# Performance work log

Measured on AMD Instinct MI355X. Metric: run time of the kernel, lower is better.

## Reference

```python
import math
import jax, jax.numpy as jnp
import numpy as np


def _skew(X, pad_value):
    # shift every row i one step right relative to row i-1: [B,M,L] -> [B,M,M+L]
    B, M, L = X.shape
    X = jnp.pad(X, ((0, 0), (0, 0), (0, M + 1)), constant_values=pad_value)
    X = X.reshape(B, -1)[:, :-M]
    return X.reshape(B, M, M + L)


def _unskew(X):
    # reverse of _skew: [B,M,M+L] -> [B,M,L]
    B, M, ML = X.shape
    L = ML - M
    X = X.reshape(B, -1)
    X = jnp.pad(X, ((0, 0), (0, M)))
    X = X.reshape(B, M, M + L + 1)
    return X[:, :, :L]


def setup_inputs() -> dict:
    key0 = jax.random.key(0)
    k1, k2, k3, k4 = jax.random.split(key0, 4)
    BH, M, D = 64, 1024, 64          # batch*heads, block len, head dim
    L = 1024                          # attn_span
    return {
        "query": jax.random.normal(k1, (BH, M, D), dtype=jnp.float32),
        "key": jax.random.normal(k2, (BH, M + L, D), dtype=jnp.float32),
        "value": jax.random.normal(k3, (BH, M + L, D), dtype=jnp.float32),
        "key_pe": jax.random.normal(k4, (1, D, L), dtype=jnp.float32),
    }


def reference(query, key, value, key_pe):
    hidden_size = query.shape[-1]
    # content scores: [BH, M, M+L] -> banded [BH, M, L]
    attn_cont = _unskew(jnp.matmul(query, jnp.swapaxes(key, -1, -2)))
    # relative position scores: [BH, M, L] (key_pe broadcasts over batch)
    attn_pos = jnp.matmul(query, key_pe)
    attn = (attn_cont + attn_pos) / math.sqrt(hidden_size)
    attn = jax.nn.softmax(attn, axis=-1)
    # dropout p=0.0 -> identity
    attn_skew = _skew(attn, 0.0)          # [BH, M, M+L]
    out = jnp.matmul(attn_skew, value)    # [BH, M, D]
    return out
```

## Files before the change

### kernel.cpp

```cpp
#include <hip/hip_runtime.h>
#include <hip/hip_bf16.h>


typedef __attribute__((ext_vector_type(8))) short bf16x8;
typedef __attribute__((ext_vector_type(4))) short bf16x4;
typedef __attribute__((ext_vector_type(4))) float f32x4;

#define BHN   64
#define MQ    1024
#define DH    64
#define LS    1024
#define NKEY  2048
#define NTILE 17

#define SZ_PE  ((size_t)LS * DH * 2)
#define OFF_K  SZ_PE
#define SZ_K   ((size_t)BHN * NKEY * DH * 2)
#define OFF_V  (OFF_K + SZ_K)
#define SZ_V   ((size_t)BHN * DH * NKEY * 2)
#define WS_NEED (OFF_V + SZ_V)

#define SCL_LOG2E 0.18033688011112042f

__device__ __forceinline__ short f2bf(float f) {
  unsigned u = __float_as_uint(f);
  u += 0x7FFFu + ((u >> 16) & 1u);
  return (short)(u >> 16);
}
__device__ __forceinline__ float bf2f(short s) {
  return __uint_as_float(((unsigned)(unsigned short)s) << 16);
}

#if defined(__has_builtin)
#if __has_builtin(__builtin_amdgcn_cvt_pk_bf16_f32)
#define HAVE_CVT_PK 1
#endif
#if __has_builtin(__builtin_amdgcn_exp2f)
#define HAVE_EXP2 1
#endif
#endif

__device__ __forceinline__ float fast_exp2(float x) {
#ifdef HAVE_EXP2
  return __builtin_amdgcn_exp2f(x);
#else
  return __builtin_exp2f(x);
#endif
}

__device__ __forceinline__ unsigned pk2(float a, float b) {
#ifdef HAVE_CVT_PK
  auto r = __builtin_amdgcn_cvt_pk_bf16_f32(a, b);
  unsigned u;
  __builtin_memcpy(&u, &r, 4);
  return u;
#else
  return (unsigned)(unsigned short)f2bf(a) | ((unsigned)(unsigned short)f2bf(b) << 16);
#endif
}
__device__ __forceinline__ bf16x4 mk4(unsigned a, unsigned b) {
  union { unsigned u[2]; bf16x4 v; } z;
  z.u[0] = a; z.u[1] = b;
  return z.v;
}
__device__ __forceinline__ bf16x8 mk8(unsigned a, unsigned b, unsigned c, unsigned d) {
  union { unsigned u[4]; bf16x8 v; } z;
  z.u[0] = a; z.u[1] = b; z.u[2] = c; z.u[3] = d;
  return z.v;
}

__global__ __launch_bounds__(256)
void prep_fused(const float* __restrict__ pe, const float* __restrict__ K,
                const float* __restrict__ V, short* __restrict__ peT,
                short* __restrict__ Kb, short* __restrict__ Vb) {
  __shared__ short st[64 * 68];
  const int bx = blockIdx.x;
  if (bx < 256) {
    const int idx = bx * 256 + threadIdx.x;
    const int rel = idx >> 6, d = idx & 63;
    peT[rel * 64 + (((d >> 3) ^ (rel & 7)) * 8) + (d & 7)] = f2bf(pe[d * LS + rel]);
  } else if (bx < 2304) {
    const size_t i = ((size_t)(bx - 256) * 256 + threadIdx.x) * 16;
    const int row = (int)(i >> 6);
    const int c16 = (int)(i & 63);
    const float4 f0 = *(const float4*)(K + i);
    const float4 f1 = *(const float4*)(K + i + 4);
    const float4 f2 = *(const float4*)(K + i + 8);
    const float4 f3 = *(const float4*)(K + i + 12);
    const bf16x8 b0 = mk8(pk2(f0.x, f0.y), pk2(f0.z, f0.w), pk2(f1.x, f1.y), pk2(f1.z, f1.w));
    const bf16x8 b1 = mk8(pk2(f2.x, f2.y), pk2(f2.z, f2.w), pk2(f3.x, f3.y), pk2(f3.z, f3.w));
    const int s7 = row & 7;
    short* dst = Kb + (size_t)row * 64;
    *(bf16x8*)&dst[(((c16 >> 3))     ^ s7) * 8] = b0;
    *(bf16x8*)&dst[(((c16 >> 3) + 1) ^ s7) * 8] = b1;
  } else {
    const int b  = bx - 2304;
    const int bh = b >> 5, jt = b & 31;
    {
      const int r = threadIdx.x >> 2, cb = (threadIdx.x & 3) * 16;
      const float* src = V + ((size_t)bh * NKEY + jt * 64 + r) * DH + cb;
#pragma unroll
      for (int c = 0; c < 16; c += 8) {
        float4 f0 = *(const float4*)(src + c);
        float4 f1 = *(const float4*)(src + c + 4);
        *(bf16x8*)&st[r * 68 + cb + c] =
            mk8(pk2(f0.x, f0.y), pk2(f0.z, f0.w), pk2(f1.x, f1.y), pk2(f1.z, f1.w));
      }
    }
    __syncthreads();
    {
      const int d = threadIdx.x >> 2, kapb = (threadIdx.x & 3) * 16;
      __attribute__((aligned(16))) short tmp[16];
#pragma unroll
      for (int j = 0; j < 16; ++j) {
        const int kap = kapb + j;
        const int k   = (kap & 3) * 16 + (kap >> 2);
        tmp[j] = st[k * 68 + d];
      }
      short* dst = Vb + ((size_t)bh * DH + d) * NKEY + jt * 64 + kapb;
      *(bf16x8*)dst       = *(bf16x8*)&tmp[0];
      *(bf16x8*)(dst + 8) = *(bf16x8*)&tmp[8];
    }
  }
}

template <bool PRECONV>
__global__ __launch_bounds__(256, 4)
void seq_attn_kernel(const float* __restrict__ Qf, const float* __restrict__ Kf,
                     const float* __restrict__ Vf, const short* __restrict__ peT,
                     const short* __restrict__ Kb, const short* __restrict__ Vb,
                     float* __restrict__ Out) {
  __shared__ short sK[64 * 64];
  __shared__ short sPE[2 * 64 * 64];
  __shared__ short sV[64 * 64];
  __shared__ short sPA[64 * 64];

  const int tid  = threadIdx.x;
  const int w    = tid >> 6;
  const int lane = tid & 63;
  const int li   = lane & 15;
  const int quad = lane >> 4;
  const int linear = blockIdx.y * 16 + blockIdx.x;
  const int slot   = linear >> 3;
  const int bh     = (linear & 7) * 8 + (slot >> 4);
  const int i0     = (slot & 15) * 64;
  const int rbase  = w * 16 + quad * 4;

  bf16x8 aq[2];
  {
    const float* qp = Qf + (size_t)((bh * MQ + i0 + w * 16 + li) * DH) + quad * 8;
#pragma unroll
    for (int ks = 0; ks < 2; ++ks) {
      float4 f0 = *(const float4*)(qp + ks * 32);
      float4 f1 = *(const float4*)(qp + ks * 32 + 4);
      f0.x *= SCL_LOG2E; f0.y *= SCL_LOG2E; f0.z *= SCL_LOG2E; f0.w *= SCL_LOG2E;
      f1.x *= SCL_LOG2E; f1.y *= SCL_LOG2E; f1.z *= SCL_LOG2E; f1.w *= SCL_LOG2E;
      aq[ks] = mk8(pk2(f0.x, f0.y), pk2(f0.z, f0.w), pk2(f1.x, f1.y), pk2(f1.z, f1.w));
    }
  }

  float l_i[4] = {0.f, 0.f, 0.f, 0.f};
  f32x4 acco[4];
#pragma unroll
  for (int nt = 0; nt < 4; ++nt) acco[nt] = (f32x4){0.f, 0.f, 0.f, 0.f};

  f32x4 curPw[4];
  f32x4 prevw3 = (f32x4){0.f, 0.f, 0.f, 0.f};

  bf16x8 pfK0, pfK1, pfP0, pfP1, pfV0, pfV1;
  const short *pK, *pP, *pV0, *pV1;
  if constexpr (PRECONV) {
    pK = Kb + ((size_t)bh * NKEY + i0) * DH + tid * 8 + 1024;
    pP = peT + tid * 8 + 1024;
    const int d0 = tid >> 3;
    const int g0 = (tid & 7) ^ (d0 & 7);
    pV0 = Vb + ((size_t)bh * DH + d0) * NKEY + i0 + g0 * 8;
    pV1 = pV0 + (size_t)32 * NKEY;
    pfK0 = *(const bf16x8*)(pK - 1024);
    pfK1 = *(const bf16x8*)(pK + 1024);
    pfP0 = *(const bf16x8*)(pP - 1024);
    pfP1 = *(const bf16x8*)(pP + 1024);
    pfV0 = *(const bf16x8*)(pV0);
    pfV1 = *(const bf16x8*)(pV1);
    pK += 4096; pP += 4096; pV0 += 64; pV1 += 64;
  }

  for (int t = 0; t < NTILE; ++t) {
    __syncthreads();

    if constexpr (PRECONV) {
      *(bf16x8*)&sK[tid * 8]        = pfK0;
      *(bf16x8*)&sK[tid * 8 + 2048] = pfK1;
      if (t < NTILE - 1) {
        short* pe = sPE + (t & 1) * 4096;
        *(bf16x8*)&pe[tid * 8]        = pfP0;
        *(bf16x8*)&pe[tid * 8 + 2048] = pfP1;
      }
      *(bf16x8*)&sV[tid * 8]        = pfV0;
      *(bf16x8*)&sV[tid * 8 + 2048] = pfV1;
      if (t + 1 < NTILE) {
        pfK0 = *(const bf16x8*)(pK - 1024);
        pfK1 = *(const bf16x8*)(pK + 1024);
        pfV0 = *(const bf16x8*)(pV0);
        pfV1 = *(const bf16x8*)(pV1);
        pK += 4096; pV0 += 64; pV1 += 64;
        if (t + 1 < NTILE - 1) {
          pfP0 = *(const bf16x8*)(pP - 1024);
          pfP1 = *(const bf16x8*)(pP + 1024);
          pP += 4096;
        }
      }
      asm volatile("s_waitcnt lgkmcnt(0)" ::: "memory");
      __builtin_amdgcn_sched_barrier(0);
      __builtin_amdgcn_s_barrier();
      __builtin_amdgcn_sched_barrier(0);
    } else {
      const int j0 = i0 + t * 64;
      {
        const int srow = tid >> 2, l0 = tid & 3, sdb = l0 * 16;
        const float* src = Kf + (size_t)(bh * NKEY + j0 + srow) * DH + sdb;
        const float4 a0 = *(const float4*)(src + 0);
        const float4 a1 = *(const float4*)(src + 4);
        const float4 a2 = *(const float4*)(src + 8);
        const float4 a3 = *(const float4*)(src + 12);
        const bf16x8 b0 = mk8(pk2(a0.x, a0.y), pk2(a0.z, a0.w), pk2(a1.x, a1.y), pk2(a1.z, a1.w));
        const bf16x8 b1 = mk8(pk2(a2.x, a2.y), pk2(a2.z, a2.w), pk2(a3.x, a3.y), pk2(a3.z, a3.w));
        const int s7 = srow & 7;
        *(bf16x8*)&sK[srow * 64 + (((2 * l0)     ^ s7) * 8)] = b0;
        *(bf16x8*)&sK[srow * 64 + (((2 * l0 + 1) ^ s7) * 8)] = b1;
      }
      {
        const int vdb = (tid & 15) * 4, vkb = (tid >> 4) * 4;
        const float* src = Vf + (size_t)(bh * NKEY + j0 + vkb) * DH + vdb;
#pragma unroll
        for (int m = 0; m < 4; ++m) {
          const float4 rr = *(const float4*)(src + m * DH);
          const int k   = vkb + m;
          const int kap = (k & 15) * 4 + (k >> 4);
#pragma unroll
          for (int jj = 0; jj < 4; ++jj) {
            const int d = vdb + jj;
            const float fv = (jj == 0) ? rr.x : (jj == 1) ? rr.y : (jj == 2) ? rr.z : rr.w;
            sV[d * 64 + (((kap >> 3) ^ (d & 7)) * 8) + (kap & 7)] = f2bf(fv);
          }
        }
      }
      if (t < NTILE - 1) {
        const short* src = peT + (size_t)t * 64 * 64;
        short* db = sPE + (size_t)(t & 1) * 4096;
        *(bf16x8*)&db[tid * 16]     = *(const bf16x8*)(src + tid * 16);
        *(bf16x8*)&db[tid * 16 + 8] = *(const bf16x8*)(src + tid * 16 + 8);
      }
      __syncthreads();
    }

    __builtin_amdgcn_s_setprio(1);
#pragma unroll
    for (int m = 0; m < 4; ++m) {
      const int colIdx = 4 * t - w + m;
      const int base = ((colIdx >> 2) & 1) * 4096 + ((colIdx & 3) * 16 + li) * 64;
      f32x4 c = (f32x4){0.f, 0.f, 0.f, 0.f};
#pragma unroll
      for (int ks = 0; ks < 2; ++ks) {
        const int gs = (((ks * 4 + quad) ^ (li & 7)) * 8);
        const bf16x8 b = *(bf16x8*)&sPE[base + gs];
        c = __builtin_amdgcn_mfma_f32_16x16x32_bf16(aq[ks], b, c, 0, 0, 0);
      }
      curPw[m] = c;
    }

    f32x4 cs[4];
#pragma unroll
    for (int nt = 0; nt < 4; ++nt) {
      f32x4 c = (f32x4){0.f, 0.f, 0.f, 0.f};
#pragma unroll
      for (int ks = 0; ks < 2; ++ks) {
        const int gs = (((ks * 4 + quad) ^ (li & 7)) * 8);
        const bf16x8 b = *(bf16x8*)&sK[(nt * 16 + li) * 64 + gs];
        c = __builtin_amdgcn_mfma_f32_16x16x32_bf16(aq[ks], b, c, 0, 0, 0);
      }
      cs[nt] = c;
    }
    __builtin_amdgcn_s_setprio(0);

#pragma unroll
    for (int r = 0; r < 4; ++r) {
      const int e       = li - quad * 4 - r;
      const bool ge     = (e >= 0);
      const int srcLane = quad * 16 + (e & 15);
      const float shm = __shfl(prevw3[r], srcLane);
      const unsigned pk01 = pk2(curPw[0][r], curPw[1][r]);
      const unsigned pk23 = pk2(curPw[2][r], curPw[3][r]);
      const unsigned s01 = (unsigned)__shfl((int)pk01, srcLane);
      const unsigned s23 = (unsigned)__shfl((int)pk23, srcLane);
      const float sh0 = bf2f((short)(s01 & 0xffffu));
      const float sh1 = bf2f((short)(s01 >> 16));
      const float sh2 = bf2f((short)(s23 & 0xffffu));
      const float sh3 = bf2f((short)(s23 >> 16));
      const float pos0 = ge ? sh0 : shm;
      const float pos1 = ge ? sh1 : sh0;
      const float pos2 = ge ? sh2 : sh1;
      const float pos3 = ge ? sh3 : sh2;
      float p0 = fast_exp2(cs[0][r] + pos0);
      float p1 = fast_exp2(cs[1][r] + pos1);
      float p2 = fast_exp2(cs[2][r] + pos2);
      float p3 = fast_exp2(cs[3][r] + pos3);
      if (t == 0) {
        p0 = (0 > w || (0 == w && ge)) ? p0 : 0.f;
        p1 = (1 > w || (1 == w && ge)) ? p1 : 0.f;
        p2 = (2 > w || (2 == w && ge)) ? p2 : 0.f;
        p3 = (3 > w || (3 == w && ge)) ? p3 : 0.f;
      } else if (t == NTILE - 1) {
        p0 = (0 < w || (0 == w && !ge)) ? p0 : 0.f;
        p1 = (1 < w || (1 == w && !ge)) ? p1 : 0.f;
        p2 = (2 < w || (2 == w && !ge)) ? p2 : 0.f;
        p3 = (3 < w || (3 == w && !ge)) ? p3 : 0.f;
      }
      l_i[r] += (p0 + p1) + (p2 + p3);
      const int rowA = rbase + r;
      const bf16x4 pkv = mk4(pk2(p0, p1), pk2(p2, p3));
      *(bf16x4*)&sPA[rowA * 64 + (((li >> 1) ^ (rowA & 7)) * 8) + (li & 1) * 4] = pkv;
    }
    prevw3 = curPw[3];

    __builtin_amdgcn_s_setprio(1);
#pragma unroll
    for (int ks = 0; ks < 2; ++ks) {
      const int rowA = w * 16 + li;
      const bf16x8 ap =
          *(bf16x8*)&sPA[rowA * 64 + (((ks * 4 + quad) ^ (rowA & 7)) * 8)];
#pragma unroll
      for (int nt = 0; nt < 4; ++nt) {
        const int d  = nt * 16 + li;
        const int gs = (((ks * 4 + quad) ^ (d & 7)) * 8);
        const bf16x8 bv = *(bf16x8*)&sV[d * 64 + gs];
        acco[nt] = __builtin_amdgcn_mfma_f32_16x16x32_bf16(ap, bv, acco[nt], 0, 0, 0);
      }
    }
    __builtin_amdgcn_s_setprio(0);
  }

#pragma unroll
  for (int r = 0; r < 4; ++r) {
    float l = l_i[r];
    l += __shfl_xor(l, 1);
    l += __shfl_xor(l, 2);
    l += __shfl_xor(l, 4);
    l += __shfl_xor(l, 8);
    const float inv = 1.0f / l;
#pragma unroll
    for (int nt = 0; nt < 4; ++nt) {
      Out[(size_t)(bh * MQ + i0 + rbase + r) * DH + nt * 16 + li] = acco[nt][r] * inv;
    }
  }
}

extern "C" void kernel_launch(void* const* d_in, const int* in_sizes, int n_in,
                              void* d_out, int out_size, void* d_ws, size_t ws_size,
                              hipStream_t stream) {
  const float* q  = (const float*)d_in[0];
  const float* k  = (const float*)d_in[1];
  const float* v  = (const float*)d_in[2];
  const float* pe = (const float*)d_in[3];
  float* out = (float*)d_out;
  short* peT = (short*)d_ws;
  short* Kb  = (short*)((char*)d_ws + OFF_K);
  short* Vb  = (short*)((char*)d_ws + OFF_V);
  const bool preconv = ws_size >= WS_NEED;

  dim3 grid(MQ / 64, BHN);
  if (preconv) {
    prep_fused<<<4352, 256, 0, stream>>>(pe, k, v, peT, Kb, Vb);
    seq_attn_kernel<true><<<grid, 256, 0, stream>>>(q, k, v, peT, Kb, Vb, out);
  } else {
    prep_fused<<<256, 256, 0, stream>>>(pe, k, v, peT, Kb, Vb);
    seq_attn_kernel<false><<<grid, 256, 0, stream>>>(q, k, v, peT, Kb, Vb, out);
  }
}
```

Before: 171.3 us.

## Process two 64-row query groups per block to reuse K/V tiles

Each block now handles 128 query rows as two 64-row groups that share every loaded K and V tile, so the band loop runs 18 tiles instead of 17 per 64 rows. This roughly halves global K/V traffic per query row. The PE buffer becomes a 4-slot ring, the P staging buffer doubles, and the barrier moves to the start of each iteration. In exchange, register pressure rises (launch bounds drop to 2 blocks per CU), the grid halves to 512 blocks, and one extra masked tile adds wasted work per group.

```diff
diff --git a/kernel.cpp b/kernel.cpp
--- a/kernel.cpp
+++ b/kernel.cpp
@@ -11,7 +11,8 @@
 #define DH    64
 #define LS    1024
 #define NKEY  2048
-#define NTILE 17
+#define NT    18
+#define NPE   16
 
 #define SZ_PE  ((size_t)LS * DH * 2)
 #define OFF_K  SZ_PE
@@ -124,48 +125,99 @@
   }
 }
 
+__device__ __forceinline__ void softmax_band(
+    const f32x4* cs, const f32x4* cur, const f32x4& prev,
+    float (&l_acc)[4], short* sPA, const int rowbase, const int tt,
+    const int w, const int li, const int quad) {
+#pragma unroll
+  for (int r = 0; r < 4; ++r) {
+    const int e       = li - quad * 4 - r;
+    const bool ge     = (e >= 0);
+    const int srcLane = quad * 16 + (e & 15);
+    const float shm = __shfl(prev[r], srcLane);
+    const unsigned pk01 = pk2(cur[0][r], cur[1][r]);
+    const unsigned pk23 = pk2(cur[2][r], cur[3][r]);
+    const unsigned s01 = (unsigned)__shfl((int)pk01, srcLane);
+    const unsigned s23 = (unsigned)__shfl((int)pk23, srcLane);
+    const float sh0 = bf2f((short)(s01 & 0xffffu));
+    const float sh1 = bf2f((short)(s01 >> 16));
+    const float sh2 = bf2f((short)(s23 & 0xffffu));
+    const float sh3 = bf2f((short)(s23 >> 16));
+    const float pos0 = ge ? sh0 : shm;
+    const float pos1 = ge ? sh1 : sh0;
+    const float pos2 = ge ? sh2 : sh1;
+    const float pos3 = ge ? sh3 : sh2;
+    float p0 = fast_exp2(cs[0][r] + pos0);
+    float p1 = fast_exp2(cs[1][r] + pos1);
+    float p2 = fast_exp2(cs[2][r] + pos2);
+    float p3 = fast_exp2(cs[3][r] + pos3);
+    if (tt == 0) {
+      p0 = (0 > w || (0 == w && ge)) ? p0 : 0.f;
+      p1 = (1 > w || (1 == w && ge)) ? p1 : 0.f;
+      p2 = (2 > w || (2 == w && ge)) ? p2 : 0.f;
+      p3 = (3 > w || (3 == w && ge)) ? p3 : 0.f;
+    } else if (tt == 16) {
+      p0 = (0 < w || (0 == w && !ge)) ? p0 : 0.f;
+      p1 = (1 < w || (1 == w && !ge)) ? p1 : 0.f;
+      p2 = (2 < w || (2 == w && !ge)) ? p2 : 0.f;
+      p3 = (3 < w || (3 == w && !ge)) ? p3 : 0.f;
+    } else if ((unsigned)tt > 16u) {
+      p0 = 0.f; p1 = 0.f; p2 = 0.f; p3 = 0.f;
+    }
+    l_acc[r] += (p0 + p1) + (p2 + p3);
+    const int rowA = rowbase + w * 16 + quad * 4 + r;
+    const bf16x4 pkv = mk4(pk2(p0, p1), pk2(p2, p3));
+    *(bf16x4*)&sPA[rowA * 64 + (((li >> 1) ^ (rowA & 7)) * 8) + (li & 1) * 4] = pkv;
+  }
+}
+
 template <bool PRECONV>
-__global__ __launch_bounds__(256, 4)
+__global__ __launch_bounds__(256, 2)
 void seq_attn_kernel(const float* __restrict__ Qf, const float* __restrict__ Kf,
                      const float* __restrict__ Vf, const short* __restrict__ peT,
                      const short* __restrict__ Kb, const short* __restrict__ Vb,
                      float* __restrict__ Out) {
   __shared__ short sK[64 * 64];
-  __shared__ short sPE[2 * 64 * 64];
+  __shared__ short sPE[4 * 64 * 64];
   __shared__ short sV[64 * 64];
-  __shared__ short sPA[64 * 64];
+  __shared__ short sPA[128 * 64];
 
   const int tid  = threadIdx.x;
   const int w    = tid >> 6;
   const int lane = tid & 63;
   const int li   = lane & 15;
   const int quad = lane >> 4;
-  const int linear = blockIdx.y * 16 + blockIdx.x;
-  const int slot   = linear >> 3;
-  const int bh     = (linear & 7) * 8 + (slot >> 4);
-  const int i0     = (slot & 15) * 64;
+  const int linear = blockIdx.y * 8 + blockIdx.x;
+  const int within = linear >> 3;
+  const int bh     = (linear & 7) * 8 + (within >> 3);
+  const int i0     = (within & 7) * 128;
   const int rbase  = w * 16 + quad * 4;
 
-  bf16x8 aq[2];
-  {
-    const float* qp = Qf + (size_t)((bh * MQ + i0 + w * 16 + li) * DH) + quad * 8;
+  bf16x8 aq0[2], aq1[2];
+#pragma unroll
+  for (int g = 0; g < 2; ++g) {
+    const float* qp = Qf + (size_t)((bh * MQ + i0 + g * 64 + w * 16 + li) * DH) + quad * 8;
 #pragma unroll
     for (int ks = 0; ks < 2; ++ks) {
       float4 f0 = *(const float4*)(qp + ks * 32);
       float4 f1 = *(const float4*)(qp + ks * 32 + 4);
       f0.x *= SCL_LOG2E; f0.y *= SCL_LOG2E; f0.z *= SCL_LOG2E; f0.w *= SCL_LOG2E;
       f1.x *= SCL_LOG2E; f1.y *= SCL_LOG2E; f1.z *= SCL_LOG2E; f1.w *= SCL_LOG2E;
-      aq[ks] = mk8(pk2(f0.x, f0.y), pk2(f0.z, f0.w), pk2(f1.x, f1.y), pk2(f1.z, f1.w));
-    }
-  }
-
-  float l_i[4] = {0.f, 0.f, 0.f, 0.f};
-  f32x4 acco[4];
-#pragma unroll
-  for (int nt = 0; nt < 4; ++nt) acco[nt] = (f32x4){0.f, 0.f, 0.f, 0.f};
-
-  f32x4 curPw[4];
-  f32x4 prevw3 = (f32x4){0.f, 0.f, 0.f, 0.f};
+      const bf16x8 v = mk8(pk2(f0.x, f0.y), pk2(f0.z, f0.w), pk2(f1.x, f1.y), pk2(f1.z, f1.w));
+      if (g == 0) aq0[ks] = v; else aq1[ks] = v;
+    }
+  }
+
+  float l0[4] = {0.f, 0.f, 0.f, 0.f};
+  float l1[4] = {0.f, 0.f, 0.f, 0.f};
+  f32x4 acco0[4], acco1[4];
+#pragma unroll
+  for (int nt = 0; nt < 4; ++nt) {
+    acco0[nt] = (f32x4){0.f, 0.f, 0.f, 0.f};
+    acco1[nt] = (f32x4){0.f, 0.f, 0.f, 0.f};
+  }
+  f32x4 prev0 = (f32x4){0.f, 0.f, 0.f, 0.f};
+  f32x4 prev1 = (f32x4){0.f, 0.f, 0.f, 0.f};
 
   bf16x8 pfK0, pfK1, pfP0, pfP1, pfV0, pfV1;
   const short *pK, *pP, *pV0, *pV1;
@@ -185,26 +237,28 @@
     pK += 4096; pP += 4096; pV0 += 64; pV1 += 64;
   }
 
-  for (int t = 0; t < NTILE; ++t) {
-    __syncthreads();
-
+  for (int t = 0; t < NT; ++t) {
     if constexpr (PRECONV) {
+      asm volatile("s_waitcnt lgkmcnt(0)" ::: "memory");
+      __builtin_amdgcn_sched_barrier(0);
+      __builtin_amdgcn_s_barrier();
+      __builtin_amdgcn_sched_barrier(0);
       *(bf16x8*)&sK[tid * 8]        = pfK0;
       *(bf16x8*)&sK[tid * 8 + 2048] = pfK1;
-      if (t < NTILE - 1) {
-        short* pe = sPE + (t & 1) * 4096;
-        *(bf16x8*)&pe[tid * 8]        = pfP0;
-        *(bf16x8*)&pe[tid * 8 + 2048] = pfP1;
+      if (t < NPE) {
+        short* ped = sPE + (size_t)(t & 3) * 4096;
+        *(bf16x8*)&ped[tid * 8]        = pfP0;
+        *(bf16x8*)&ped[tid * 8 + 2048] = pfP1;
       }
       *(bf16x8*)&sV[tid * 8]        = pfV0;
       *(bf16x8*)&sV[tid * 8 + 2048] = pfV1;
-      if (t + 1 < NTILE) {
+      if (t + 1 < NT) {
         pfK0 = *(const bf16x8*)(pK - 1024);
         pfK1 = *(const bf16x8*)(pK + 1024);
         pfV0 = *(const bf16x8*)(pV0);
         pfV1 = *(const bf16x8*)(pV1);
         pK += 4096; pV0 += 64; pV1 += 64;
-        if (t + 1 < NTILE - 1) {
+        if (t + 1 < NPE) {
           pfP0 = *(const bf16x8*)(pP - 1024);
           pfP1 = *(const bf16x8*)(pP + 1024);
           pP += 4096;
@@ -215,9 +269,10 @@
       __builtin_amdgcn_s_barrier();
       __builtin_amdgcn_sched_barrier(0);
     } else {
+      __syncthreads();
       const int j0 = i0 + t * 64;
       {
-        const int srow = tid >> 2, l0 = tid & 3, sdb = l0 * 16;
+        const int srow = tid >> 2, lx = tid & 3, sdb = lx * 16;
         const float* src = Kf + (size_t)(bh * NKEY + j0 + srow) * DH + sdb;
         const float4 a0 = *(const float4*)(src + 0);
         const float4 a1 = *(const float4*)(src + 4);
@@ -226,8 +281,8 @@
         const bf16x8 b0 = mk8(pk2(a0.x, a0.y), pk2(a0.z, a0.w), pk2(a1.x, a1.y), pk2(a1.z, a1.w));
         const bf16x8 b1 = mk8(pk2(a2.x, a2.y), pk2(a2.z, a2.w), pk2(a3.x, a3.y), pk2(a3.z, a3.w));
         const int s7 = srow & 7;
-        *(bf16x8*)&sK[srow * 64 + (((2 * l0)     ^ s7) * 8)] = b0;
-        *(bf16x8*)&sK[srow * 64 + (((2 * l0 + 1) ^ s7) * 8)] = b1;
+        *(bf16x8*)&sK[srow * 64 + (((2 * lx)     ^ s7) * 8)] = b0;
+        *(bf16x8*)&sK[srow * 64 + (((2 * lx + 1) ^ s7) * 8)] = b1;
       }
       {
         const int vdb = (tid & 15) * 4, vkb = (tid >> 4) * 4;
@@ -245,96 +300,79 @@
           }
         }
       }
-      if (t < NTILE - 1) {
+      if (t < NPE) {
         const short* src = peT + (size_t)t * 64 * 64;
-        short* db = sPE + (size_t)(t & 1) * 4096;
+        short* db = sPE + (size_t)(t & 3) * 4096;
         *(bf16x8*)&db[tid * 16]     = *(const bf16x8*)(src + tid * 16);
         *(bf16x8*)&db[tid * 16 + 8] = *(const bf16x8*)(src + tid * 16 + 8);
       }
       __syncthreads();
     }
 
+    f32x4 cur0[4], cur1[4];
     __builtin_amdgcn_s_setprio(1);
 #pragma unroll
     for (int m = 0; m < 4; ++m) {
       const int colIdx = 4 * t - w + m;
-      const int base = ((colIdx >> 2) & 1) * 4096 + ((colIdx & 3) * 16 + li) * 64;
+      const int base = ((colIdx >> 2) & 3) * 4096 + ((colIdx & 3) * 16 + li) * 64;
       f32x4 c = (f32x4){0.f, 0.f, 0.f, 0.f};
 #pragma unroll
       for (int ks = 0; ks < 2; ++ks) {
         const int gs = (((ks * 4 + quad) ^ (li & 7)) * 8);
         const bf16x8 b = *(bf16x8*)&sPE[base + gs];
-        c = __builtin_amdgcn_mfma_f32_16x16x32_bf16(aq[ks], b, c, 0, 0, 0);
-      }
-      curPw[m] = c;
-    }
-
-    f32x4 cs[4];
+        c = __builtin_amdgcn_mfma_f32_16x16x32_bf16(aq0[ks], b, c, 0, 0, 0);
+      }
+      cur0[m] = c;
+    }
+#pragma unroll
+    for (int m = 0; m < 4; ++m) {
+      const int colIdx = 4 * t - w + m - 4;
+      const int base = ((colIdx >> 2) & 3) * 4096 + ((colIdx & 3) * 16 + li) * 64;
+      f32x4 c = (f32x4){0.f, 0.f, 0.f, 0.f};
+#pragma unroll
+      for (int ks = 0; ks < 2; ++ks) {
+        const int gs = (((ks * 4 + quad) ^ (li & 7)) * 8);
+        const bf16x8 b = *(bf16x8*)&sPE[base + gs];
+        c = __builtin_amdgcn_mfma_f32_16x16x32_bf16(aq1[ks], b, c, 0, 0, 0);
+      }
+      cur1[m] = c;
+    }
+
+    f32x4 cs0[4], cs1[4];
 #pragma unroll
     for (int nt = 0; nt < 4; ++nt) {
-      f32x4 c = (f32x4){0.f, 0.f, 0.f, 0.f};
+      f32x4 c0 = (f32x4){0.f, 0.f, 0.f, 0.f};
+      f32x4 c1 = (f32x4){0.f, 0.f, 0.f, 0.f};
 #pragma unroll
       for (int ks = 0; ks < 2; ++ks) {
         const int gs = (((ks * 4 + quad) ^ (li & 7)) * 8);
         const bf16x8 b = *(bf16x8*)&sK[(nt * 16 + li) * 64 + gs];
-        c = __builtin_amdgcn_mfma_f32_16x16x32_bf16(aq[ks], b, c, 0, 0, 0);
-      }
-      cs[nt] = c;
+        c0 = __builtin_amdgcn_mfma_f32_16x16x32_bf16(aq0[ks], b, c0, 0, 0, 0);
+        c1 = __builtin_amdgcn_mfma_f32_16x16x32_bf16(aq1[ks], b, c1, 0, 0, 0);
+      }
+      cs0[nt] = c0; cs1[nt] = c1;
     }
     __builtin_amdgcn_s_setprio(0);
 
-#pragma unroll
-    for (int r = 0; r < 4; ++r) {
-      const int e       = li - quad * 4 - r;
-      const bool ge     = (e >= 0);
-      const int srcLane = quad * 16 + (e & 15);
-      const float shm = __shfl(prevw3[r], srcLane);
-      const unsigned pk01 = pk2(curPw[0][r], curPw[1][r]);
-      const unsigned pk23 = pk2(curPw[2][r], curPw[3][r]);
-      const unsigned s01 = (unsigned)__shfl((int)pk01, srcLane);
-      const unsigned s23 = (unsigned)__shfl((int)pk23, srcLane);
-      const float sh0 = bf2f((short)(s01 & 0xffffu));
-      const float sh1 = bf2f((short)(s01 >> 16));
-      const float sh2 = bf2f((short)(s23 & 0xffffu));
-      const float sh3 = bf2f((short)(s23 >> 16));
-      const float pos0 = ge ? sh0 : shm;
-      const float pos1 = ge ? sh1 : sh0;
-      const float pos2 = ge ? sh2 : sh1;
-      const float pos3 = ge ? sh3 : sh2;
-      float p0 = fast_exp2(cs[0][r] + pos0);
-      float p1 = fast_exp2(cs[1][r] + pos1);
-      float p2 = fast_exp2(cs[2][r] + pos2);
-      float p3 = fast_exp2(cs[3][r] + pos3);
-      if (t == 0) {
-        p0 = (0 > w || (0 == w && ge)) ? p0 : 0.f;
-        p1 = (1 > w || (1 == w && ge)) ? p1 : 0.f;
-        p2 = (2 > w || (2 == w && ge)) ? p2 : 0.f;
-        p3 = (3 > w || (3 == w && ge)) ? p3 : 0.f;
-      } else if (t == NTILE - 1) {
-        p0 = (0 < w || (0 == w && !ge)) ? p0 : 0.f;
-        p1 = (1 < w || (1 == w && !ge)) ? p1 : 0.f;
-        p2 = (2 < w || (2 == w && !ge)) ? p2 : 0.f;
-        p3 = (3 < w || (3 == w && !ge)) ? p3 : 0.f;
-      }
-      l_i[r] += (p0 + p1) + (p2 + p3);
-      const int rowA = rbase + r;
-      const bf16x4 pkv = mk4(pk2(p0, p1), pk2(p2, p3));
-      *(bf16x4*)&sPA[rowA * 64 + (((li >> 1) ^ (rowA & 7)) * 8) + (li & 1) * 4] = pkv;
-    }
-    prevw3 = curPw[3];
+    softmax_band(cs0, cur0, prev0, l0, sPA, 0,  t,     w, li, quad);
+    softmax_band(cs1, cur1, prev1, l1, sPA, 64, t - 1, w, li, quad);
+    prev0 = cur0[3];
+    prev1 = cur1[3];
 
     __builtin_amdgcn_s_setprio(1);
 #pragma unroll
     for (int ks = 0; ks < 2; ++ks) {
-      const int rowA = w * 16 + li;
-      const bf16x8 ap =
-          *(bf16x8*)&sPA[rowA * 64 + (((ks * 4 + quad) ^ (rowA & 7)) * 8)];
+      const int rA0 = w * 16 + li;
+      const int rA1 = rA0 + 64;
+      const bf16x8 ap0 = *(bf16x8*)&sPA[rA0 * 64 + (((ks * 4 + quad) ^ (rA0 & 7)) * 8)];
+      const bf16x8 ap1 = *(bf16x8*)&sPA[rA1 * 64 + (((ks * 4 + quad) ^ (rA1 & 7)) * 8)];
 #pragma unroll
       for (int nt = 0; nt < 4; ++nt) {
         const int d  = nt * 16 + li;
         const int gs = (((ks * 4 + quad) ^ (d & 7)) * 8);
         const bf16x8 bv = *(bf16x8*)&sV[d * 64 + gs];
-        acco[nt] = __builtin_amdgcn_mfma_f32_16x16x32_bf16(ap, bv, acco[nt], 0, 0, 0);
+        acco0[nt] = __builtin_amdgcn_mfma_f32_16x16x32_bf16(ap0, bv, acco0[nt], 0, 0, 0);
+        acco1[nt] = __builtin_amdgcn_mfma_f32_16x16x32_bf16(ap1, bv, acco1[nt], 0, 0, 0);
       }
     }
     __builtin_amdgcn_s_setprio(0);
@@ -342,7 +380,7 @@
 
 #pragma unroll
   for (int r = 0; r < 4; ++r) {
-    float l = l_i[r];
+    float l = l0[r];
     l += __shfl_xor(l, 1);
     l += __shfl_xor(l, 2);
     l += __shfl_xor(l, 4);
@@ -350,7 +388,20 @@
     const float inv = 1.0f / l;
 #pragma unroll
     for (int nt = 0; nt < 4; ++nt) {
-      Out[(size_t)(bh * MQ + i0 + rbase + r) * DH + nt * 16 + li] = acco[nt][r] * inv;
+      Out[(size_t)(bh * MQ + i0 + rbase + r) * DH + nt * 16 + li] = acco0[nt][r] * inv;
+    }
+  }
+#pragma unroll
+  for (int r = 0; r < 4; ++r) {
+    float l = l1[r];
+    l += __shfl_xor(l, 1);
+    l += __shfl_xor(l, 2);
+    l += __shfl_xor(l, 4);
+    l += __shfl_xor(l, 8);
+    const float inv = 1.0f / l;
+#pragma unroll
+    for (int nt = 0; nt < 4; ++nt) {
+      Out[(size_t)(bh * MQ + i0 + 64 + rbase + r) * DH + nt * 16 + li] = acco1[nt][r] * inv;
     }
   }
 }
@@ -368,7 +419,7 @@
   short* Vb  = (short*)((char*)d_ws + OFF_V);
   const bool preconv = ws_size >= WS_NEED;
 
-  dim3 grid(MQ / 64, BHN);
+  dim3 grid(8, BHN);
   if (preconv) {
     prep_fused<<<4352, 256, 0, stream>>>(pe, k, v, peT, Kb, Vb);
     seq_attn_kernel<true><<<grid, 256, 0, stream>>>(q, k, v, peT, Kb, Vb, out);
```

Measured after the change: 175.4 us. 2.4% more time.

## Software-pipeline QK of next tile with softmax/PV of previous, drop PE LDS staging

Applied to the files above, without the earlier changes.

Restructures the main loop into two-tile steps so the QK and position-score MFMAs for one tile are issued before the softmax and PV of the previous tile, giving cross-tile overlap. The position-embedding B operand is now read straight from global memory (peT) instead of being staged in LDS, and the P matrix reuses the sK buffer. V is double-buffered instead. The exchange is more barriers per tile, higher register pressure from two live score sets, and uncoalesced-ish global reads of peT that rely on the cache.

```diff
diff --git a/kernel.cpp b/kernel.cpp
--- a/kernel.cpp
+++ b/kernel.cpp
@@ -68,6 +68,14 @@
   z.u[0] = a; z.u[1] = b; z.u[2] = c; z.u[3] = d;
   return z.v;
 }
+
+#define RAWBAR()                                          \
+  do {                                                    \
+    asm volatile("s_waitcnt lgkmcnt(0)" ::: "memory");    \
+    __builtin_amdgcn_sched_barrier(0);                    \
+    __builtin_amdgcn_s_barrier();                         \
+    __builtin_amdgcn_sched_barrier(0);                    \
+  } while (0)
 
 __global__ __launch_bounds__(256)
 void prep_fused(const float* __restrict__ pe, const float* __restrict__ K,
@@ -124,6 +132,110 @@
   }
 }
 
+__device__ __forceinline__ void qk_tile(const short* sK, const bf16x8 (&aq)[2],
+                                        int li, int quad, f32x4 (&cs)[4]) {
+  const int g0 = ((quad) ^ (li & 7)) * 8;
+  const int g1 = ((4 + quad) ^ (li & 7)) * 8;
+#pragma unroll
+  for (int nt = 0; nt < 4; ++nt) {
+    const int row = (nt * 16 + li) * 64;
+    f32x4 c = (f32x4){0.f, 0.f, 0.f, 0.f};
+    c = __builtin_amdgcn_mfma_f32_16x16x32_bf16(aq[0], *(const bf16x8*)&sK[row + g0], c, 0, 0, 0);
+    c = __builtin_amdgcn_mfma_f32_16x16x32_bf16(aq[1], *(const bf16x8*)&sK[row + g1], c, 0, 0, 0);
+    cs[nt] = c;
+  }
+}
+
+__device__ __forceinline__ void pe_tile(const short* __restrict__ peT,
+                                        const bf16x8 (&aq)[2], int t, int w,
+                                        int li, int quad, unsigned (&pk)[8]) {
+  const int g0 = ((quad) ^ (li & 7)) * 8;
+  const int g1 = ((4 + quad) ^ (li & 7)) * 8;
+  f32x4 cur[4];
+#pragma unroll
+  for (int m = 0; m < 4; ++m) {
+    int cidx = 4 * t - w + m;
+    cidx = cidx < 0 ? 0 : (cidx > 63 ? 63 : cidx);
+    const short* p = peT + (size_t)(cidx * 16 + li) * 64;
+    f32x4 c = (f32x4){0.f, 0.f, 0.f, 0.f};
+    c = __builtin_amdgcn_mfma_f32_16x16x32_bf16(aq[0], *(const bf16x8*)(p + g0), c, 0, 0, 0);
+    c = __builtin_amdgcn_mfma_f32_16x16x32_bf16(aq[1], *(const bf16x8*)(p + g1), c, 0, 0, 0);
+    cur[m] = c;
+  }
+#pragma unroll
+  for (int r = 0; r < 4; ++r) {
+    pk[r * 2]     = pk2(cur[0][r], cur[1][r]);
+    pk[r * 2 + 1] = pk2(cur[2][r], cur[3][r]);
+  }
+}
+
+__device__ __forceinline__ void softmax_tile(const f32x4 (&cs)[4], const unsigned (&pk)[8],
+                                             f32x4& prevw3, float (&l_i)[4],
+                                             bf16x4 (&pkv)[4], int tt, int w,
+                                             int li, int quad) {
+#pragma unroll
+  for (int r = 0; r < 4; ++r) {
+    const int e       = li - quad * 4 - r;
+    const bool ge     = (e >= 0);
+    const int srcLane = quad * 16 + (e & 15);
+    const float shm = __shfl(prevw3[r], srcLane);
+    const unsigned s01 = (unsigned)__shfl((int)pk[r * 2], srcLane);
+    const unsigned s23 = (unsigned)__shfl((int)pk[r * 2 + 1], srcLane);
+    const float sh0 = bf2f((short)(s01 & 0xffffu));
+    const float sh1 = bf2f((short)(s01 >> 16));
+    const float sh2 = bf2f((short)(s23 & 0xffffu));
+    const float sh3 = bf2f((short)(s23 >> 16));
+    const float pos0 = ge ? sh0 : shm;
+    const float pos1 = ge ? sh1 : sh0;
+    const float pos2 = ge ? sh2 : sh1;
+    const float pos3 = ge ? sh3 : sh2;
+    float p0 = fast_exp2(cs[0][r] + pos0);
+    float p1 = fast_exp2(cs[1][r] + pos1);
+    float p2 = fast_exp2(cs[2][r] + pos2);
+    float p3 = fast_exp2(cs[3][r] + pos3);
+    if (tt == 0) {
+      p0 = (0 > w || (0 == w && ge)) ? p0 : 0.f;
+      p1 = (1 > w || (1 == w && ge)) ? p1 : 0.f;
+      p2 = (2 > w || (2 == w && ge)) ? p2 : 0.f;
+      p3 = (3 > w || (3 == w && ge)) ? p3 : 0.f;
+    } else if (tt == NTILE - 1) {
+      p0 = (0 < w || (0 == w && !ge)) ? p0 : 0.f;
+      p1 = (1 < w || (1 == w && !ge)) ? p1 : 0.f;
+      p2 = (2 < w || (2 == w && !ge)) ? p2 : 0.f;
+      p3 = (3 < w || (3 == w && !ge)) ? p3 : 0.f;
+    }
+    l_i[r] += (p0 + p1) + (p2 + p3);
+    pkv[r] = mk4(pk2(p0, p1), pk2(p2, p3));
+  }
+#pragma unroll
+  for (int r = 0; r < 4; ++r) prevw3[r] = bf2f((short)(pk[r * 2 + 1] >> 16));
+}
+
+__device__ __forceinline__ void pv_tile(short* sP, const short* sV,
+                                        const bf16x4 (&pkv)[4], f32x4 (&acco)[4],
+                                        int w, int li, int quad) {
+  const int rbase = w * 16 + quad * 4;
+#pragma unroll
+  for (int r = 0; r < 4; ++r) {
+    const int rowA = rbase + r;
+    *(bf16x4*)&sP[rowA * 64 + (((li >> 1) ^ (rowA & 7)) * 8) + (li & 1) * 4] = pkv[r];
+  }
+  const int rowA = w * 16 + li;
+  __builtin_amdgcn_s_setprio(1);
+#pragma unroll
+  for (int ks = 0; ks < 2; ++ks) {
+    const bf16x8 ap = *(const bf16x8*)&sP[rowA * 64 + (((ks * 4 + quad) ^ (rowA & 7)) * 8)];
+#pragma unroll
+    for (int nt = 0; nt < 4; ++nt) {
+      const int d  = nt * 16 + li;
+      const int gs = (((ks * 4 + quad) ^ (d & 7)) * 8);
+      const bf16x8 bv = *(const bf16x8*)&sV[d * 64 + gs];
+      acco[nt] = __builtin_amdgcn_mfma_f32_16x16x32_bf16(ap, bv, acco[nt], 0, 0, 0);
+    }
+  }
+  __builtin_amdgcn_s_setprio(0);
+}
+
 template <bool PRECONV>
 __global__ __launch_bounds__(256, 4)
 void seq_attn_kernel(const float* __restrict__ Qf, const float* __restrict__ Kf,
@@ -131,9 +243,7 @@
                      const short* __restrict__ Kb, const short* __restrict__ Vb,
                      float* __restrict__ Out) {
   __shared__ short sK[64 * 64];
-  __shared__ short sPE[2 * 64 * 64];
-  __shared__ short sV[64 * 64];
-  __shared__ short sPA[64 * 64];
+  __shared__ short sV[2 * 64 * 64];
 
   const int tid  = threadIdx.x;
   const int w    = tid >> 6;
@@ -163,58 +273,77 @@
   f32x4 acco[4];
 #pragma unroll
   for (int nt = 0; nt < 4; ++nt) acco[nt] = (f32x4){0.f, 0.f, 0.f, 0.f};
-
-  f32x4 curPw[4];
   f32x4 prevw3 = (f32x4){0.f, 0.f, 0.f, 0.f};
 
-  bf16x8 pfK0, pfK1, pfP0, pfP1, pfV0, pfV1;
-  const short *pK, *pP, *pV0, *pV1;
   if constexpr (PRECONV) {
+    bf16x8 pfK0, pfK1, pfV0, pfV1;
+    const short *pK, *pV0, *pV1;
     pK = Kb + ((size_t)bh * NKEY + i0) * DH + tid * 8 + 1024;
-    pP = peT + tid * 8 + 1024;
-    const int d0 = tid >> 3;
-    const int g0 = (tid & 7) ^ (d0 & 7);
-    pV0 = Vb + ((size_t)bh * DH + d0) * NKEY + i0 + g0 * 8;
-    pV1 = pV0 + (size_t)32 * NKEY;
+    {
+      const int d0 = tid >> 3;
+      const int g0 = (tid & 7) ^ (d0 & 7);
+      pV0 = Vb + ((size_t)bh * DH + d0) * NKEY + i0 + g0 * 8;
+      pV1 = pV0 + (size_t)32 * NKEY;
+    }
     pfK0 = *(const bf16x8*)(pK - 1024);
     pfK1 = *(const bf16x8*)(pK + 1024);
-    pfP0 = *(const bf16x8*)(pP - 1024);
-    pfP1 = *(const bf16x8*)(pP + 1024);
     pfV0 = *(const bf16x8*)(pV0);
     pfV1 = *(const bf16x8*)(pV1);
-    pK += 4096; pP += 4096; pV0 += 64; pV1 += 64;
-  }
-
-  for (int t = 0; t < NTILE; ++t) {
-    __syncthreads();
-
-    if constexpr (PRECONV) {
-      *(bf16x8*)&sK[tid * 8]        = pfK0;
-      *(bf16x8*)&sK[tid * 8 + 2048] = pfK1;
-      if (t < NTILE - 1) {
-        short* pe = sPE + (t & 1) * 4096;
-        *(bf16x8*)&pe[tid * 8]        = pfP0;
-        *(bf16x8*)&pe[tid * 8 + 2048] = pfP1;
+    pK += 4096; pV0 += 64; pV1 += 64;
+
+    f32x4 csE[4], csO[4];
+    unsigned pkE[8], pkO[8];
+    bf16x4 pkv[4];
+
+#define STAGE_PF(VSLOT, HAVE_NEXT)                                         \
+    do {                                                                   \
+      *(bf16x8*)&sK[tid * 8]        = pfK0;                                \
+      *(bf16x8*)&sK[tid * 8 + 2048] = pfK1;                                \
+      short* sv = sV + (VSLOT) * 4096;                                     \
+      *(bf16x8*)&sv[tid * 8]        = pfV0;                                \
+      *(bf16x8*)&sv[tid * 8 + 2048] = pfV1;                                \
+      if (HAVE_NEXT) {                                                     \
+        pfK0 = *(const bf16x8*)(pK - 1024);                                \
+        pfK1 = *(const bf16x8*)(pK + 1024);                                \
+        pfV0 = *(const bf16x8*)(pV0);                                      \
+        pfV1 = *(const bf16x8*)(pV1);                                      \
+        pK += 4096; pV0 += 64; pV1 += 64;                                  \
+      }                                                                    \
+    } while (0)
+
+    for (int tb = 0; tb < 9; ++tb) {
+      const int t0 = 2 * tb;
+      RAWBAR();
+      STAGE_PF(0, tb < 8);
+      RAWBAR();
+      __builtin_amdgcn_s_setprio(1);
+      qk_tile(sK, aq, li, quad, csE);
+      pe_tile(peT, aq, t0, w, li, quad, pkE);
+      __builtin_amdgcn_s_setprio(0);
+      if (tb > 0)
+        softmax_tile(csO, pkO, prevw3, l_i, pkv, t0 - 1, w, li, quad);
+      RAWBAR();
+      if (tb > 0)
+        pv_tile(sK, sV + 4096, pkv, acco, w, li, quad);
+
+      const int t1 = t0 + 1;
+      if (tb < 8) {
+        RAWBAR();
+        STAGE_PF(1, t1 + 1 < NTILE);
+        RAWBAR();
+        __builtin_amdgcn_s_setprio(1);
+        qk_tile(sK, aq, li, quad, csO);
+        pe_tile(peT, aq, t1, w, li, quad, pkO);
+        __builtin_amdgcn_s_setprio(0);
       }
-      *(bf16x8*)&sV[tid * 8]        = pfV0;
-      *(bf16x8*)&sV[tid * 8 + 2048] = pfV1;
-      if (t + 1 < NTILE) {
-        pfK0 = *(const bf16x8*)(pK - 1024);
-        pfK1 = *(const bf16x8*)(pK + 1024);
-        pfV0 = *(const bf16x8*)(pV0);
-        pfV1 = *(const bf16x8*)(pV1);
-        pK += 4096; pV0 += 64; pV1 += 64;
-        if (t + 1 < NTILE - 1) {
-          pfP0 = *(const bf16x8*)(pP - 1024);
-          pfP1 = *(const bf16x8*)(pP + 1024);
-          pP += 4096;
-        }
-      }
-      asm volatile("s_waitcnt lgkmcnt(0)" ::: "memory");
-      __builtin_amdgcn_sched_barrier(0);
-      __builtin_amdgcn_s_barrier();
-      __builtin_amdgcn_sched_barrier(0);
-    } else {
+      softmax_tile(csE, pkE, prevw3, l_i, pkv, t0, w, li, quad);
+      RAWBAR();
+      pv_tile(sK, sV, pkv, acco, w, li, quad);
+    }
+#undef STAGE_PF
+  } else {
+    for (int t = 0; t < NTILE; ++t) {
+      __syncthreads();
       const int j0 = i0 + t * 64;
       {
         const int srow = tid >> 2, l0 = tid & 3, sdb = l0 * 16;
@@ -245,99 +374,17 @@
           }
         }
       }
-      if (t < NTILE - 1) {
-        const short* src = peT + (size_t)t * 64 * 64;
-        short* db = sPE + (size_t)(t & 1) * 4096;
-        *(bf16x8*)&db[tid * 16]     = *(const bf16x8*)(src + tid * 16);
-        *(bf16x8*)&db[tid * 16 + 8] = *(const bf16x8*)(src + tid * 16 + 8);
-      }
       __syncthreads();
-    }
-
-    __builtin_amdgcn_s_setprio(1);
-#pragma unroll
-    for (int m = 0; m < 4; ++m) {
-      const int colIdx = 4 * t - w + m;
-      const int base = ((colIdx >> 2) & 1) * 4096 + ((colIdx & 3) * 16 + li) * 64;
-      f32x4 c = (f32x4){0.f, 0.f, 0.f, 0.f};
-#pragma unroll
-      for (int ks = 0; ks < 2; ++ks) {
-        const int gs = (((ks * 4 + quad) ^ (li & 7)) * 8);
-        const bf16x8 b = *(bf16x8*)&sPE[base + gs];
-        c = __builtin_amdgcn_mfma_f32_16x16x32_bf16(aq[ks], b, c, 0, 0, 0);
-      }
-      curPw[m] = c;
-    }
-
-    f32x4 cs[4];
-#pragma unroll
-    for (int nt = 0; nt < 4; ++nt) {
-      f32x4 c = (f32x4){0.f, 0.f, 0.f, 0.f};
-#pragma unroll
-      for (int ks = 0; ks < 2; ++ks) {
-        const int gs = (((ks * 4 + quad) ^ (li & 7)) * 8);
-        const bf16x8 b = *(bf16x8*)&sK[(nt * 16 + li) * 64 + gs];
-        c = __builtin_amdgcn_mfma_f32_16x16x32_bf16(aq[ks], b, c, 0, 0, 0);
-      }
-      cs[nt] = c;
-    }
-    __builtin_amdgcn_s_setprio(0);
-
-#pragma unroll
-    for (int r = 0; r < 4; ++r) {
-      const int e       = li - quad * 4 - r;
-      const bool ge     = (e >= 0);
-      const int srcLane = quad * 16 + (e & 15);
-      const float shm = __shfl(prevw3[r], srcLane);
-      const unsigned pk01 = pk2(curPw[0][r], curPw[1][r]);
-      const unsigned pk23 = pk2(curPw[2][r], curPw[3][r]);
-      const unsigned s01 = (unsigned)__shfl((int)pk01, srcLane);
-      const unsigned s23 = (unsigned)__shfl((int)pk23, srcLane);
-      const float sh0 = bf2f((short)(s01 & 0xffffu));
-      const float sh1 = bf2f((short)(s01 >> 16));
-      const float sh2 = bf2f((short)(s23 & 0xffffu));
-      const float sh3 = bf2f((short)(s23 >> 16));
-      const float pos0 = ge ? sh0 : shm;
-      const float pos1 = ge ? sh1 : sh0;
-      const float pos2 = ge ? sh2 : sh1;
-      const float pos3 = ge ? sh3 : sh2;
-      float p0 = fast_exp2(cs[0][r] + pos0);
-      float p1 = fast_exp2(cs[1][r] + pos1);
-      float p2 = fast_exp2(cs[2][r] + pos2);
-      float p3 = fast_exp2(cs[3][r] + pos3);
-      if (t == 0) {
-        p0 = (0 > w || (0 == w && ge)) ? p0 : 0.f;
-        p1 = (1 > w || (1 == w && ge)) ? p1 : 0.f;
-        p2 = (2 > w || (2 == w && ge)) ? p2 : 0.f;
-        p3 = (3 > w || (3 == w && ge)) ? p3 : 0.f;
-      } else if (t == NTILE - 1) {
-        p0 = (0 < w || (0 == w && !ge)) ? p0 : 0.f;
-        p1 = (1 < w || (1 == w && !ge)) ? p1 : 0.f;
-        p2 = (2 < w || (2 == w && !ge)) ? p2 : 0.f;
-        p3 = (3 < w || (3 == w && !ge)) ? p3 : 0.f;
-      }
-      l_i[r] += (p0 + p1) + (p2 + p3);
-      const int rowA = rbase + r;
-      const bf16x4 pkv = mk4(pk2(p0, p1), pk2(p2, p3));
-      *(bf16x4*)&sPA[rowA * 64 + (((li >> 1) ^ (rowA & 7)) * 8) + (li & 1) * 4] = pkv;
-    }
-    prevw3 = curPw[3];
-
-    __builtin_amdgcn_s_setprio(1);
-#pragma unroll
-    for (int ks = 0; ks < 2; ++ks) {
-      const int rowA = w * 16 + li;
-      const bf16x8 ap =
-          *(bf16x8*)&sPA[rowA * 64 + (((ks * 4 + quad) ^ (rowA & 7)) * 8)];
-#pragma unroll
-      for (int nt = 0; nt < 4; ++nt) {
-        const int d  = nt * 16 + li;
-        const int gs = (((ks * 4 + quad) ^ (d & 7)) * 8);
-        const bf16x8 bv = *(bf16x8*)&sV[d * 64 + gs];
-        acco[nt] = __builtin_amdgcn_mfma_f32_16x16x32_bf16(ap, bv, acco[nt], 0, 0, 0);
-      }
-    }
-    __builtin_amdgcn_s_setprio(0);
+
+      f32x4 cs[4];
+      unsigned pk[8];
+      bf16x4 pkv[4];
+      qk_tile(sK, aq, li, quad, cs);
+      pe_tile(peT, aq, t, w, li, quad, pk);
+      softmax_tile(cs, pk, prevw3, l_i, pkv, t, w, li, quad);
+      __syncthreads();
+      pv_tile(sK, sV, pkv, acco, w, li, quad);
+    }
   }
 
 #pragma unroll
```

New measurement: 287.9 us. +68.1%, slower.
